# Kernel optimization log

Measured on AMD Instinct MI355X. Metric: run time of the kernel, lower is better.

The kernel has to match this reference:

```python
import jax, jax.numpy as jnp
import numpy as np
from jax import lax

NEG = -1e30  # log-space -inf surrogate

def setup_inputs() -> dict:
    key = jax.random.key(0)
    ks = jax.random.split(key, 6)
    B, T, D, V, Lmax = 16, 800, 512, 4000, 100
    hs_pad = jax.random.normal(ks[0], (B, T, D), dtype=jnp.float32)
    W = jax.random.normal(ks[1], (D, V), dtype=jnp.float32) * 0.02
    b = jnp.zeros((V,), dtype=jnp.float32)
    hlens = jax.random.randint(ks[2], (B,), 400, T + 1, dtype=jnp.int32)
    ys_pad = jax.random.randint(ks[3], (B, Lmax), 1, V, dtype=jnp.int32)
    ys_lens = jax.random.randint(ks[4], (B,), 50, Lmax + 1, dtype=jnp.int32)
    return {"hs_pad": hs_pad, "W": W, "b": b, "hlens": hlens,
            "ys_pad": ys_pad, "ys_lens": ys_lens}

def _ctc_loss(lp, ys_pad, hlens, ys_lens):
    # lp: [T, B, V] log-probs; blank = 0
    T, B, V = lp.shape
    Lmax = ys_pad.shape[1]
    S = 2 * Lmax + 1  # extended label length: blank-interleaved
    ext = jnp.zeros((B, S), dtype=ys_pad.dtype).at[:, 1::2].set(ys_pad)
    # skip transition s-2 -> s allowed when ext[s] != blank and ext[s] != ext[s-2]
    skip = jnp.concatenate(
        [jnp.zeros((B, 2), dtype=bool),
         (ext[:, 2:] != 0) & (ext[:, 2:] != ext[:, :-2])], axis=1)
    # per-frame emission log-probs for extended labels: [T, B, S]
    emit = jnp.take_along_axis(lp, jnp.broadcast_to(ext[None], (T, B, S)), axis=2)
    alpha0 = jnp.full((B, S), NEG, dtype=lp.dtype).at[:, :2].set(emit[0, :, :2])

    def step(alpha, inp):
        emit_t, active = inp  # [B, S], [B]
        s1 = jnp.pad(alpha[:, :-1], ((0, 0), (1, 0)), constant_values=NEG)
        s2 = jnp.pad(alpha[:, :-2], ((0, 0), (2, 0)), constant_values=NEG)
        s2 = jnp.where(skip, s2, NEG)
        new = jnp.logaddexp(jnp.logaddexp(alpha, s1), s2) + emit_t
        alpha = jnp.where(active[:, None], new, alpha)  # freeze past hlen
        return alpha, None

    active = jnp.arange(1, T)[:, None] < hlens[None, :]  # [T-1, B]
    alpha, _ = lax.scan(step, alpha0, (emit[1:], active))
    idx = (2 * ys_lens).astype(jnp.int32)  # last blank position
    a_last = jnp.take_along_axis(alpha, idx[:, None], axis=1)[:, 0]
    a_prev = jnp.take_along_axis(alpha, (idx - 1)[:, None], axis=1)[:, 0]
    loss = -jnp.logaddexp(a_last, a_prev)
    # zero_infinity=True
    return jnp.where(jnp.isfinite(loss) & (loss < 1e29), loss, 0.0)

def reference(hs_pad, W, b, hlens, ys_pad, ys_lens):
    # ctc_lo projection (dropout_rate=0.0) -> [T, B, V] -> log_softmax
    logits = jnp.einsum('btd,dv->btv', hs_pad, W) + b
    lp = jax.nn.log_softmax(logits, axis=-1).transpose(1, 0, 2)
    loss = _ctc_loss(lp, ys_pad, hlens, ys_lens)
    B = hs_pad.shape[0]
    return loss.sum() / B  # reduce=True: sum / batch size
```

## Files before the change

### kernel.cpp

```cpp
#include <hip/hip_runtime.h>
#include <hip/hip_bf16.h>
#include <math.h>

#define NEGV -1e30f
#define LN2F 0.6931471805599453f


typedef __attribute__((ext_vector_type(8))) short bf16x8;
typedef __attribute__((ext_vector_type(4))) float f32x4;

__device__ __forceinline__ short f2bf(float x) {
    __hip_bfloat16 h = __float2bfloat16(x);
    return __builtin_bit_cast(short, h);
}

__device__ __forceinline__ float shup1(float x) {
    return __builtin_bit_cast(float,
        __builtin_amdgcn_update_dpp(0, __builtin_bit_cast(int, x),
                                    0x138, 0xf, 0xf, true));
}

#define GLD_LDS(g, l) \
    __builtin_amdgcn_global_load_lds( \
        (const __attribute__((address_space(1))) void*)(g), \
        (__attribute__((address_space(3))) void*)(l), 16, 0, 0)

#define WAITV(n) do { \
    asm volatile("s_waitcnt vmcnt(" #n ")" ::: "memory"); \
    __builtin_amdgcn_sched_barrier(0); \
} while (0)

__global__ __launch_bounds__(256) void prep(
    const float* __restrict__ hs, const float* __restrict__ W,
    const float* __restrict__ bias, const int* __restrict__ ys,
    short* __restrict__ W2, short* __restrict__ A2,
    float* __restrict__ biasp, unsigned char* __restrict__ M,
    unsigned char* __restrict__ canon, float* __restrict__ lse_sum,
    float* __restrict__ out)
{
    __shared__ float tile[32][65];
    __shared__ unsigned char mapl[4096];
    const int bx = blockIdx.x, tid = threadIdx.x;

    if (bx < 1024) {
        const int n0 = (bx & 63) * 64;
        const int k0 = (bx >> 6) * 32;
        #pragma unroll
        for (int p = 0; p < 8; p++) {
            int idx = p * 256 + tid;
            int k = idx >> 6, n = idx & 63;
            int gn = n0 + n;
            tile[k][n] = (gn < 4000) ? W[(size_t)(k0 + k) * 4000 + gn] : 0.0f;
        }
        __syncthreads();
        const int nn = tid >> 6, lane = tid & 63;
        const int l16 = lane & 15, quad = lane >> 4;
        const int ct = n0 >> 7, wn = (n0 >> 6) & 1, it = k0 >> 5;
        size_t chunk = ((((size_t)ct * 16 + it) * 2 + wn) * 4 + nn) * 64 + lane;
        bf16x8 r;
        #pragma unroll
        for (int j = 0; j < 8; j++) r[j] = f2bf(tile[quad * 8 + j][nn * 16 + l16]);
        *(bf16x8*)(W2 + chunk * 8) = r;
    } else if (bx < 4224) {
        int g = (bx - 1024) * 256 + tid;
        int lane = g & 63, mi = (g >> 6) & 3, wm = (g >> 8) & 1;
        int it = (g >> 9) & 15, rb = g >> 13;
        int row = rb * 128 + wm * 64 + mi * 16 + (lane & 15);
        int k = it * 32 + (lane >> 4) * 8;
        const float* src = hs + (size_t)row * 512 + k;
        float4 u = *(const float4*)src;
        float4 v = *(const float4*)(src + 4);
        bf16x8 r;
        r[0] = f2bf(u.x); r[1] = f2bf(u.y); r[2] = f2bf(u.z); r[3] = f2bf(u.w);
        r[4] = f2bf(v.x); r[5] = f2bf(v.y); r[6] = f2bf(v.z); r[7] = f2bf(v.w);
        *(bf16x8*)(A2 + (size_t)g * 8) = r;
    } else {
        for (int b = 0; b < 16; b++) {
            for (int i = tid; i < 1024; i += 256)
                ((unsigned int*)mapl)[i] = 0xFFFFFFFFu;
            __syncthreads();
            if (tid == 0) mapl[0] = 0;
            __syncthreads();
            if (tid < 100) mapl[ys[b * 100 + tid]] = (unsigned char)(tid + 1);
            __syncthreads();
            for (int i = tid; i < 1024; i += 256)
                ((unsigned int*)(M + (size_t)b * 4096))[i] = ((const unsigned int*)mapl)[i];
            if (tid < 128) {
                int colc = (tid >= 1 && tid <= 100) ? ys[b * 100 + tid - 1] : 0;
                canon[b * 128 + tid] = mapl[colc];
            }
            __syncthreads();
        }
        for (int i = tid; i < 4096; i += 256)
            biasp[i] = (i < 4000) ? bias[i] : NEGV;
        for (int i = tid; i < 12800; i += 256)
            lse_sum[i] = 0.0f;
        if (tid == 0) out[0] = 0.0f;
    }
}

__global__ __launch_bounds__(512, 4) void lse_mfma(
    const short* __restrict__ A2,
    const short* __restrict__ W2,
    const float* __restrict__ biasp,
    const unsigned char* __restrict__ M,
    float* __restrict__ lse_sum,
    __hip_bfloat16* __restrict__ Praw)
{
    const unsigned int bid = blockIdx.x;
    const unsigned int xcd = bid & 7;
    const unsigned int s = bid >> 3;
    const unsigned int cp = s / 13;
    const unsigned int rl = s - cp * 13;
    const unsigned int rb = rl * 8 + xcd;
    if (rb >= 100) return;

    const int tid = threadIdx.x;
    const int w = tid >> 6, lane = tid & 63;
    const int quad = lane >> 4, l16 = lane & 15;
    const int wm = w >> 2;
    const int wc = w & 3;
    const int row0 = rb * 128;
    const int col0 = cp * 256;

    __shared__ __align__(16) short sbuf[3][12288];

    const short* gb[3];
    int lo[3];
    #pragma unroll
    for (int j = 0; j < 3; j++) {
        int sg = 3 * w + j;
        const short* cbase =
            (sg < 8)  ? (A2 + (size_t)rb * 65536)
          : (sg < 16) ? (W2 + (size_t)(2 * cp) * 65536)
                      : (W2 + (size_t)(2 * cp + 1) * 65536);
        gb[j] = cbase + (sg & 7) * 512 + lane * 8;
        lo[j] = sg * 512 + lane * 8;
    }

#define STAGE(s_, bi_) do { \
    GLD_LDS(gb[0] + (size_t)(s_) * 4096, &sbuf[bi_][lo[0]]); \
    GLD_LDS(gb[1] + (size_t)(s_) * 4096, &sbuf[bi_][lo[1]]); \
    GLD_LDS(gb[2] + (size_t)(s_) * 4096, &sbuf[bi_][lo[2]]); \
} while (0)

    f32x4 acc[4][4];
    #pragma unroll
    for (int mi = 0; mi < 4; mi++)
        #pragma unroll
        for (int ni = 0; ni < 4; ni++) acc[mi][ni] = (f32x4){0.f,0.f,0.f,0.f};

    STAGE(0, 0);
    STAGE(1, 1);
    WAITV(3);
    __builtin_amdgcn_s_barrier();
    __builtin_amdgcn_sched_barrier(0);

    const int boff = 4096 + (wc >> 1) * 4096 + (wc & 1) * 2048;

    #pragma unroll
    for (int it = 0; it < 16; ++it) {
        if (it + 2 < 16) STAGE(it + 2, (it + 2) % 3);

        const short* cb = &sbuf[it % 3][0];
        const short* ap = cb + wm * 2048 + lane * 8;
        const short* bp = cb + boff + lane * 8;
        bf16x8 af[4], bfr[4];
        #pragma unroll
        for (int mi = 0; mi < 4; mi++) af[mi]  = *(const bf16x8*)(ap + mi * 512);
        #pragma unroll
        for (int ni = 0; ni < 4; ni++) bfr[ni] = *(const bf16x8*)(bp + ni * 512);

        __builtin_amdgcn_s_setprio(1);
        #pragma unroll
        for (int mi = 0; mi < 4; mi++)
            #pragma unroll
            for (int ni = 0; ni < 4; ni++)
                acc[mi][ni] = __builtin_amdgcn_mfma_f32_16x16x32_bf16(
                    af[mi], bfr[ni], acc[mi][ni], 0, 0, 0);
        __builtin_amdgcn_s_setprio(0);

        if (it < 15) {
            if (it < 14) { WAITV(3); }
            else         { WAITV(0); }
            __builtin_amdgcn_s_barrier();
            __builtin_amdgcn_sched_barrier(0);
        }
    }
#undef STAGE
    __builtin_amdgcn_sched_barrier(0);

    const int b0i = row0 / 800;
    const int b1i = (b0i + 1 < 16) ? b0i + 1 : 15;
    const int bbound = (b0i + 1) * 800;
    float sv[16];
    #pragma unroll
    for (int i = 0; i < 16; i++) sv[i] = 0.0f;
    #pragma unroll
    for (int ni = 0; ni < 4; ni++) {
        int col = col0 + wc * 64 + ni * 16 + l16;
        float bj = biasp[col];
        unsigned char sl0 = M[(size_t)b0i * 4096 + col];
        unsigned char sl1 = M[(size_t)b1i * 4096 + col];
        #pragma unroll
        for (int mi = 0; mi < 4; mi++) {
            #pragma unroll
            for (int r = 0; r < 4; r++) {
                int row = row0 + wm * 64 + mi * 16 + quad * 4 + r;
                float v = acc[mi][ni][r] + bj;
                sv[mi * 4 + r] += __expf(v);
                unsigned char sl = (row < bbound) ? sl0 : sl1;
                if (sl != 255)
                    Praw[(size_t)row * 128 + sl] = __float2bfloat16(v);
            }
        }
    }
    #pragma unroll
    for (int off = 1; off < 16; off <<= 1)
        #pragma unroll
        for (int i = 0; i < 16; i++) sv[i] += __shfl_xor(sv[i], off);
    if (l16 == 0) {
        #pragma unroll
        for (int mi = 0; mi < 4; mi++)
            #pragma unroll
            for (int r = 0; r < 4; r++)
                atomicAdd(&lse_sum[row0 + wm * 64 + mi * 16 + quad * 4 + r],
                          sv[mi * 4 + r]);
    }
}

__global__ __launch_bounds__(256) void pexp(
    const __hip_bfloat16* __restrict__ Praw,
    const float* __restrict__ lse_sum,
    const unsigned char* __restrict__ canon,
    float* __restrict__ PE)
{
    __shared__ unsigned char st[224];
    __shared__ float scs[16];
    const int bp = blockIdx.x;
    const int b = bp / 50, rr = bp - b * 50;
    const int tid = threadIdx.x;
    const unsigned char* cb = canon + b * 128;
    if (tid < 224) {
        int idx = (tid + 1) >> 1;
        st[tid] = (tid & 1) ? cb[idx < 128 ? idx : 127] : (unsigned char)0;
    }
    const int row0 = b * 800 + rr * 16;
    if (tid < 16) scs[tid] = __builtin_amdgcn_rcpf(lse_sum[row0 + tid]) * 2048.0f;
    __syncthreads();
    for (int item = tid; item < 832; item += 256) {
        int i = item / 52, sg = item - i * 52;
        int row = row0 + i;
        const __hip_bfloat16* pr = Praw + (size_t)row * 128;
        float sc = scs[i];
        int s0 = sg * 4;
        float4 o;
        o.x = (s0 + 0 <= 200) ? __expf(__bfloat162float(pr[st[s0 + 0]])) * sc : 0.f;
        o.y = (s0 + 1 <= 200) ? __expf(__bfloat162float(pr[st[s0 + 1]])) * sc : 0.f;
        o.z = (s0 + 2 <= 200) ? __expf(__bfloat162float(pr[st[s0 + 2]])) * sc : 0.f;
        o.w = (s0 + 3 <= 200) ? __expf(__bfloat162float(pr[st[s0 + 3]])) * sc : 0.f;
        *(float4*)&PE[(size_t)row * 208 + s0] = o;
    }
}

__global__ __launch_bounds__(256) void ctc_dp(
    const float* __restrict__ PE,
    const int* __restrict__ hlens,
    const int* __restrict__ ys,
    const int* __restrict__ ylens,
    float* __restrict__ out)
{
    const int b = blockIdx.x, tid = threadIdx.x;
    const int w = tid >> 6, lane = tid & 63;
    __shared__ float emS[3][13376];
    __shared__ float sA[256];

    const float* Pb = PE + (size_t)b * 800 * 208;
    const int hl = hlens[b], L = ylens[b];
    const int t_stop = hl - 1;
    const int C = (t_stop + 63) >> 6;

    const int yb = b * 100;
    float kA = 0.f, kB = 0.f, kH = 0.f;
    if (lane >= 1 && 2 * lane <= 99)
        kA = (ys[yb + 2 * lane] != ys[yb + 2 * lane - 1]) ? 1.f : 0.f;
    if (2 * lane + 1 <= 99)
        kB = (ys[yb + 2 * lane + 1] != ys[yb + 2 * lane]) ? 1.f : 0.f;
    if (lane >= 1 && 2 * lane - 1 <= 99)
        kH = (ys[yb + 2 * lane - 1] != ys[yb + 2 * lane - 2]) ? 1.f : 0.f;
    const float m0  = (lane <= 50) ? 1.f : 0.f;
    const float m13 = (lane <= 49) ? 1.f : 0.f;

    float a0 = 0.f, a1 = 0.f, a2 = 0.f, a3 = 0.f;
    if (w == 0 && lane == 0) {
        a0 = Pb[0];
        a1 = Pb[1];
    }
    int kacc = 0;

#define STAGE_DP(nc_) do { \
    const char* _src = (const char*)(Pb + (size_t)(64 * (nc_) + 1) * 208); \
    char* _dst = (char*)&emS[(nc_) % 3][0]; \
    const int _base = tid - 64; \
    _Pragma("unroll") \
    for (int _j = 0; _j < 17; _j++) { \
        int _idx = _base + 192 * _j; \
        GLD_LDS(_src + (size_t)_idx * 16, _dst + (size_t)_idx * 16); \
    } \
    if (w == 1) { \
        int _idx = 3264 + lane; \
        GLD_LDS(_src + (size_t)_idx * 16, _dst + (size_t)_idx * 16); \
    } \
} while (0)

#define WAITCHUNK() do { \
    if (w == 1) { WAITV(18); } else { WAITV(17); } \
} while (0)

    if (w > 0) {
        STAGE_DP(0);
        STAGE_DP(1);
        WAITCHUNK();
    }
    __builtin_amdgcn_s_barrier();
    __builtin_amdgcn_sched_barrier(0);

    for (int ch = 0; ch < C; ch++) {
        if (w > 0) {
            if (ch + 2 < C) {
                STAGE_DP(ch + 2);
                WAITCHUNK();
            } else {
                WAITV(0);
            }
        } else {
            const float* bb = emS[ch % 3];
            const int t0 = 64 * ch + 1;
            const int soff = 4 * lane;
            if (t0 + 63 <= t_stop) {
                f32x4 e = *(const f32x4*)&bb[0 * 208 + soff];
                f32x4 f = *(const f32x4*)&bb[1 * 208 + soff];
                #pragma unroll
                for (int k = 0; k < 32; k++) {
                    f32x4 en = (f32x4){0.f,0.f,0.f,0.f};
                    f32x4 fn = (f32x4){0.f,0.f,0.f,0.f};
                    if (k < 31) {
                        en = *(const f32x4*)&bb[(2 * k + 2) * 208 + soff];
                        fn = *(const f32x4*)&bb[(2 * k + 3) * 208 + soff];
                    }
                    float pht = shup1(e[3]);
                    float h1 = shup1(a3);
                    float h2 = shup1(a2);
                    float h3 = shup1(a1);
                    float tm1 = fmaf(kH, h3, h1 + h2);
                    float t0v = a0 + h1;
                    float t1v = fmaf(kA, h1, a1 + a0);
                    float t2v = a2 + a1;
                    float t3v = fmaf(kB, a1, a3 + a2);
                    float um1 = pht * tm1;
                    float u0 = e[0] * t0v, u1 = e[1] * t1v;
                    float u2 = e[2] * t2v, u3 = e[3] * t3v;
                    a0 = (f[0] * (u0 + um1)) * m0;
                    a1 = (f[1] * fmaf(kA, um1, u1 + u0)) * m13;
                    a2 = (f[2] * (u2 + u1)) * m13;
                    a3 = (f[3] * fmaf(kB, u1, u3 + u2)) * m13;
                    if ((k & 7) == 7) {
                        int tc = t0 + 2 * k + 1;
                        float lm = fmaxf(fmaxf(a0, a1), fmaxf(a2, a3));
                        int sa1 = (2 * L < tc) ? 2 * L : tc;
                        int sa2 = (int)(2.0f * L * tc / hl);
                        float v1 = __shfl(lm, sa1 >> 2);
                        float v2 = __shfl(lm, sa2 >> 2);
                        float av = fmaxf(v1, v2);
                        int eb = (__float_as_int(av) >> 23) & 0xFF;
                        if (eb != 0 && eb != 255) {
                            int e2i = eb - 127;
                            kacc += e2i;
                            float sc = __int_as_float((127 - e2i) << 23);
                            a0 *= sc; a1 *= sc; a2 *= sc; a3 *= sc;
                        }
                    }
                    e = en; f = fn;
                }
            } else {
                for (int t = t0; t <= t_stop; t++) {
                    if ((t & 15) == 0) {
                        float lm = fmaxf(fmaxf(a0, a1), fmaxf(a2, a3));
                        int sa1 = (2 * L < t) ? 2 * L : t;
                        int sa2 = (int)(2.0f * L * t / hl);
                        float v1 = __shfl(lm, sa1 >> 2);
                        float v2 = __shfl(lm, sa2 >> 2);
                        float av = fmaxf(v1, v2);
                        int eb = (__float_as_int(av) >> 23) & 0xFF;
                        if (eb != 0 && eb != 255) {
                            int e2i = eb - 127;
                            kacc += e2i;
                            float sc = __int_as_float((127 - e2i) << 23);
                            a0 *= sc; a1 *= sc; a2 *= sc; a3 *= sc;
                        }
                    }
                    f32x4 e = *(const f32x4*)&bb[(t - t0) * 208 + soff];
                    float p3 = shup1(a3);
                    float n0 = (a0 + p3) * e[0];
                    float n1 = fmaf(kA, p3, a1 + a0) * e[1];
                    float n2 = (a2 + a1) * e[2];
                    float n3 = fmaf(kB, a1, a3 + a2) * e[3];
                    a0 = n0 * m0; a1 = n1 * m13; a2 = n2 * m13; a3 = n3 * m13;
                }
            }
        }
        __builtin_amdgcn_s_barrier();
        __builtin_amdgcn_sched_barrier(0);
    }
#undef STAGE_DP
#undef WAITCHUNK

    if (w == 0) {
        sA[lane * 4 + 0] = a0; sA[lane * 4 + 1] = a1;
        sA[lane * 4 + 2] = a2; sA[lane * 4 + 3] = a3;
    }
    __syncthreads();

    if (tid == 0) {
        int idx = 2 * L;
        float s = sA[idx] + sA[idx - 1];
        float la = __logf(s) + (float)(kacc - 11 * hl) * LN2F;
        float loss = -la;
        if (!isfinite(loss) || loss >= 1e29f) loss = 0.0f;
        atomicAdd(out, loss * 0.0625f);
    }
}

extern "C" void kernel_launch(void* const* d_in, const int* in_sizes, int n_in,
                              void* d_out, int out_size, void* d_ws, size_t ws_size,
                              hipStream_t stream)
{
    const float* hs    = (const float*)d_in[0];
    const float* W     = (const float*)d_in[1];
    const float* bias  = (const float*)d_in[2];
    const int*   hlens = (const int*)d_in[3];
    const int*   ys    = (const int*)d_in[4];
    const int*   ylens = (const int*)d_in[5];
    float* out = (float*)d_out;

    char* wsb = (char*)d_ws;
    short* W2      = (short*)(wsb);
    short* A2      = (short*)(wsb + 4194304);
    float* PE      = (float*)(wsb + 4194304);
    float* biasp   = (float*)(wsb + 17301504);
    __hip_bfloat16* Praw = (__hip_bfloat16*)(wsb + 17317888);
    float* lse_sum = (float*)(wsb + 20594688);
    unsigned char* M     = (unsigned char*)(wsb + 20645888);
    unsigned char* canon = (unsigned char*)(wsb + 20711424);

    hipLaunchKernelGGL(prep,     dim3(4225), dim3(256), 0, stream,
                       hs, W, bias, ys, W2, A2, biasp, M, canon, lse_sum, out);
    hipLaunchKernelGGL(lse_mfma, dim3(1664), dim3(512), 0, stream,
                       A2, W2, biasp, M, lse_sum, Praw);
    hipLaunchKernelGGL(pexp,     dim3(800),  dim3(256), 0, stream,
                       Praw, lse_sum, canon, PE);
    hipLaunchKernelGGL(ctc_dp,   dim3(16),   dim3(256), 0, stream,
                       PE, hlens, ys, ylens, out);
}
```

Baseline: 214.6 us.

## Switch logits GEMM from bf16 to fp8 with scaled weights

Converts hs and W to FP8 (W pre-scaled by 32, result rescaled by 1/32) instead of bf16, and uses fp8 MFMA with 64-wide K stages, halving GEMM operand bytes and staging iterations. The prep kernel's label-map work is also split across 16 parallel blocks instead of one serial loop. FP8 precision loss in the logits may affect loss accuracy.

```diff
diff --git a/kernel.cpp b/kernel.cpp
--- a/kernel.cpp
+++ b/kernel.cpp
@@ -8,10 +8,18 @@
 
 typedef __attribute__((ext_vector_type(8))) short bf16x8;
 typedef __attribute__((ext_vector_type(4))) float f32x4;
+typedef __attribute__((ext_vector_type(2))) long longx2;
 
 __device__ __forceinline__ short f2bf(float x) {
     __hip_bfloat16 h = __float2bfloat16(x);
     return __builtin_bit_cast(short, h);
+}
+
+__device__ __forceinline__ int pk4(float a, float b, float c, float d) {
+    int v = 0;
+    v = __builtin_amdgcn_cvt_pk_fp8_f32(a, b, v, false);
+    v = __builtin_amdgcn_cvt_pk_fp8_f32(c, d, v, true);
+    return v;
 }
 
 __device__ __forceinline__ float shup1(float x) {
@@ -38,59 +46,73 @@
     unsigned char* __restrict__ canon, float* __restrict__ lse_sum,
     float* __restrict__ out)
 {
-    __shared__ float tile[32][65];
+    __shared__ float tile[64][65];
     __shared__ unsigned char mapl[4096];
     const int bx = blockIdx.x, tid = threadIdx.x;
 
-    if (bx < 1024) {
-        const int n0 = (bx & 63) * 64;
-        const int k0 = (bx >> 6) * 32;
-        #pragma unroll
-        for (int p = 0; p < 8; p++) {
-            int idx = p * 256 + tid;
+    if (bx < 512) {
+        const int n0g = bx & 63;
+        const int p   = bx >> 6;
+        const int k0  = p * 64;
+        #pragma unroll
+        for (int q = 0; q < 16; q++) {
+            int idx = q * 256 + tid;
             int k = idx >> 6, n = idx & 63;
-            int gn = n0 + n;
-            tile[k][n] = (gn < 4000) ? W[(size_t)(k0 + k) * 4000 + gn] : 0.0f;
+            int gn = n0g * 64 + n;
+            tile[k][n] = (gn < 4000) ? W[(size_t)(k0 + k) * 4000 + gn] * 32.0f
+                                     : 0.0f;
         }
         __syncthreads();
         const int nn = tid >> 6, lane = tid & 63;
         const int l16 = lane & 15, quad = lane >> 4;
-        const int ct = n0 >> 7, wn = (n0 >> 6) & 1, it = k0 >> 5;
-        size_t chunk = ((((size_t)ct * 16 + it) * 2 + wn) * 4 + nn) * 64 + lane;
-        bf16x8 r;
-        #pragma unroll
-        for (int j = 0; j < 8; j++) r[j] = f2bf(tile[quad * 8 + j][nn * 16 + l16]);
-        *(bf16x8*)(W2 + chunk * 8) = r;
-    } else if (bx < 4224) {
-        int g = (bx - 1024) * 256 + tid;
+        const int ct = n0g >> 1, wn = n0g & 1;
+        const int c = nn * 16 + l16;
+        float f0[8], f1[8];
+        #pragma unroll
+        for (int j = 0; j < 8; j++) {
+            f0[j] = tile[quad * 8 + j][c];
+            f1[j] = tile[32 + quad * 8 + j][c];
+        }
+        int4 o;
+        o.x = pk4(f0[0], f0[1], f0[2], f0[3]);
+        o.y = pk4(f0[4], f0[5], f0[6], f0[7]);
+        o.z = pk4(f1[0], f1[1], f1[2], f1[3]);
+        o.w = pk4(f1[4], f1[5], f1[6], f1[7]);
+        size_t chunk = ((((size_t)ct * 8 + p) * 2 + wn) * 4 + nn) * 64 + lane;
+        *(int4*)(W2 + chunk * 8) = o;
+    } else if (bx < 2112) {
+        int g = (bx - 512) * 256 + tid;
         int lane = g & 63, mi = (g >> 6) & 3, wm = (g >> 8) & 1;
-        int it = (g >> 9) & 15, rb = g >> 13;
+        int p = (g >> 9) & 7, rb = g >> 12;
         int row = rb * 128 + wm * 64 + mi * 16 + (lane & 15);
-        int k = it * 32 + (lane >> 4) * 8;
-        const float* src = hs + (size_t)row * 512 + k;
-        float4 u = *(const float4*)src;
-        float4 v = *(const float4*)(src + 4);
-        bf16x8 r;
-        r[0] = f2bf(u.x); r[1] = f2bf(u.y); r[2] = f2bf(u.z); r[3] = f2bf(u.w);
-        r[4] = f2bf(v.x); r[5] = f2bf(v.y); r[6] = f2bf(v.z); r[7] = f2bf(v.w);
-        *(bf16x8*)(A2 + (size_t)g * 8) = r;
+        int kb = p * 64 + (lane >> 4) * 8;
+        const float* src = hs + (size_t)row * 512 + kb;
+        float4 u  = *(const float4*)src;
+        float4 v  = *(const float4*)(src + 4);
+        float4 u2 = *(const float4*)(src + 32);
+        float4 v2 = *(const float4*)(src + 36);
+        int4 o;
+        o.x = pk4(u.x,  u.y,  u.z,  u.w);
+        o.y = pk4(v.x,  v.y,  v.z,  v.w);
+        o.z = pk4(u2.x, u2.y, u2.z, u2.w);
+        o.w = pk4(v2.x, v2.y, v2.z, v2.w);
+        *(int4*)(A2 + (size_t)g * 8) = o;
+    } else if (bx < 2128) {
+        const int b = bx - 2112;
+        for (int i = tid; i < 1024; i += 256)
+            ((unsigned int*)mapl)[i] = 0xFFFFFFFFu;
+        __syncthreads();
+        if (tid == 0) mapl[0] = 0;
+        __syncthreads();
+        if (tid < 100) mapl[ys[b * 100 + tid]] = (unsigned char)(tid + 1);
+        __syncthreads();
+        for (int i = tid; i < 1024; i += 256)
+            ((unsigned int*)(M + (size_t)b * 4096))[i] = ((const unsigned int*)mapl)[i];
+        if (tid < 128) {
+            int colc = (tid >= 1 && tid <= 100) ? ys[b * 100 + tid - 1] : 0;
+            canon[b * 128 + tid] = mapl[colc];
+        }
     } else {
-        for (int b = 0; b < 16; b++) {
-            for (int i = tid; i < 1024; i += 256)
-                ((unsigned int*)mapl)[i] = 0xFFFFFFFFu;
-            __syncthreads();
-            if (tid == 0) mapl[0] = 0;
-            __syncthreads();
-            if (tid < 100) mapl[ys[b * 100 + tid]] = (unsigned char)(tid + 1);
-            __syncthreads();
-            for (int i = tid; i < 1024; i += 256)
-                ((unsigned int*)(M + (size_t)b * 4096))[i] = ((const unsigned int*)mapl)[i];
-            if (tid < 128) {
-                int colc = (tid >= 1 && tid <= 100) ? ys[b * 100 + tid - 1] : 0;
-                canon[b * 128 + tid] = mapl[colc];
-            }
-            __syncthreads();
-        }
         for (int i = tid; i < 4096; i += 256)
             biasp[i] = (i < 4000) ? bias[i] : NEGV;
         for (int i = tid; i < 12800; i += 256)
@@ -131,17 +153,17 @@
     for (int j = 0; j < 3; j++) {
         int sg = 3 * w + j;
         const short* cbase =
-            (sg < 8)  ? (A2 + (size_t)rb * 65536)
-          : (sg < 16) ? (W2 + (size_t)(2 * cp) * 65536)
-                      : (W2 + (size_t)(2 * cp + 1) * 65536);
+            (sg < 8)  ? (A2 + (size_t)rb * 32768)
+          : (sg < 16) ? (W2 + (size_t)(2 * cp) * 32768)
+                      : (W2 + (size_t)(2 * cp + 1) * 32768);
         gb[j] = cbase + (sg & 7) * 512 + lane * 8;
         lo[j] = sg * 512 + lane * 8;
     }
 
-#define STAGE(s_, bi_) do { \
-    GLD_LDS(gb[0] + (size_t)(s_) * 4096, &sbuf[bi_][lo[0]]); \
-    GLD_LDS(gb[1] + (size_t)(s_) * 4096, &sbuf[bi_][lo[1]]); \
-    GLD_LDS(gb[2] + (size_t)(s_) * 4096, &sbuf[bi_][lo[2]]); \
+#define STAGE(p_, bi_) do { \
+    GLD_LDS(gb[0] + (size_t)(p_) * 4096, &sbuf[bi_][lo[0]]); \
+    GLD_LDS(gb[1] + (size_t)(p_) * 4096, &sbuf[bi_][lo[1]]); \
+    GLD_LDS(gb[2] + (size_t)(p_) * 4096, &sbuf[bi_][lo[2]]); \
 } while (0)
 
     f32x4 acc[4][4];
@@ -159,30 +181,36 @@
     const int boff = 4096 + (wc >> 1) * 4096 + (wc & 1) * 2048;
 
     #pragma unroll
-    for (int it = 0; it < 16; ++it) {
-        if (it + 2 < 16) STAGE(it + 2, (it + 2) % 3);
-
-        const short* cb = &sbuf[it % 3][0];
+    for (int p = 0; p < 8; ++p) {
+        if (p + 2 < 8) STAGE(p + 2, (p + 2) % 3);
+
+        const short* cb = &sbuf[p % 3][0];
         const short* ap = cb + wm * 2048 + lane * 8;
         const short* bp = cb + boff + lane * 8;
-        bf16x8 af[4], bfr[4];
-        #pragma unroll
-        for (int mi = 0; mi < 4; mi++) af[mi]  = *(const bf16x8*)(ap + mi * 512);
-        #pragma unroll
-        for (int ni = 0; ni < 4; ni++) bfr[ni] = *(const bf16x8*)(bp + ni * 512);
+        longx2 af[4], bf[4];
+        #pragma unroll
+        for (int mi = 0; mi < 4; mi++) af[mi] = *(const longx2*)(ap + mi * 512);
+        #pragma unroll
+        for (int ni = 0; ni < 4; ni++) bf[ni] = *(const longx2*)(bp + ni * 512);
 
         __builtin_amdgcn_s_setprio(1);
         #pragma unroll
         for (int mi = 0; mi < 4; mi++)
             #pragma unroll
             for (int ni = 0; ni < 4; ni++)
-                acc[mi][ni] = __builtin_amdgcn_mfma_f32_16x16x32_bf16(
-                    af[mi], bfr[ni], acc[mi][ni], 0, 0, 0);
+                acc[mi][ni] = __builtin_amdgcn_mfma_f32_16x16x32_fp8_fp8(
+                    af[mi][0], bf[ni][0], acc[mi][ni], 0, 0, 0);
+        #pragma unroll
+        for (int mi = 0; mi < 4; mi++)
+            #pragma unroll
+            for (int ni = 0; ni < 4; ni++)
+                acc[mi][ni] = __builtin_amdgcn_mfma_f32_16x16x32_fp8_fp8(
+                    af[mi][1], bf[ni][1], acc[mi][ni], 0, 0, 0);
         __builtin_amdgcn_s_setprio(0);
 
-        if (it < 15) {
-            if (it < 14) { WAITV(3); }
-            else         { WAITV(0); }
+        if (p < 7) {
+            if (p < 6) { WAITV(3); }
+            else       { WAITV(0); }
             __builtin_amdgcn_s_barrier();
             __builtin_amdgcn_sched_barrier(0);
         }
@@ -207,7 +235,7 @@
             #pragma unroll
             for (int r = 0; r < 4; r++) {
                 int row = row0 + wm * 64 + mi * 16 + quad * 4 + r;
-                float v = acc[mi][ni][r] + bj;
+                float v = acc[mi][ni][r] * 0.03125f + bj;
                 sv[mi * 4 + r] += __expf(v);
                 unsigned char sl = (row < bbound) ? sl0 : sl1;
                 if (sl != 255)
@@ -453,7 +481,7 @@
     unsigned char* M     = (unsigned char*)(wsb + 20645888);
     unsigned char* canon = (unsigned char*)(wsb + 20711424);
 
-    hipLaunchKernelGGL(prep,     dim3(4225), dim3(256), 0, stream,
+    hipLaunchKernelGGL(prep,     dim3(2129), dim3(256), 0, stream,
                        hs, W, bias, ys, W2, A2, biasp, M, canon, lse_sum, out);
     hipLaunchKernelGGL(lse_mfma, dim3(1664), dim3(512), 0, stream,
                        A2, W2, biasp, M, lse_sum, Praw);
```

Result: faster. 179.9 us (-16.2%).
